# Performance work log

Hardware: AMD Instinct MI355X
Metric: run time of the kernel (lower is better)

Reference implementation:

```python
import jax, jax.numpy as jnp
import numpy as np

WBITS = 4   # weight bits (symmetric signed)
ABITS = 4   # activation bits (unsigned, [0,1])
CBITS = 4   # partial-sum quantization bits
ARRAY = 128 # crossbar array size (input-dim tile)
BN_EPS = 1e-5


def ste_round(x):
    # straight-through estimator round (identity gradient)
    return x + jax.lax.stop_gradient(jnp.round(x) - x)


def setup_inputs() -> dict:
    key = jax.random.key(0)
    k1, k2 = jax.random.split(key)
    B, FIN, FOUT = 65536, 256, 256
    x = jax.random.uniform(k1, (B, FIN), dtype=jnp.float32)        # quantized-act range [0,1]
    weight = jax.random.normal(k2, (FOUT, FIN), dtype=jnp.float32) * 0.05
    gamma = jnp.ones((FOUT,), jnp.float32)
    beta = jnp.zeros((FOUT,), jnp.float32)
    return {"x": x, "weight": weight, "gamma": gamma, "beta": beta}


def reference(x, weight, gamma, beta):
    qmax_w = 2 ** (WBITS - 1) - 1          # 7
    qmax_a = 2 ** ABITS - 1                # 15

    # --- symmetric weight quantization to WBITS (integer levels) ---
    scale_w = jnp.max(jnp.abs(weight)) / qmax_w
    w_int = ste_round(jnp.clip(weight / scale_w, -qmax_w, qmax_w))  # [Fout, Fin]

    # --- unsigned activation quantization to ABITS (integer levels) ---
    x_int = ste_round(jnp.clip(x, 0.0, 1.0) * qmax_a)               # [B, Fin]

    # --- crossbar-tiled integer matmul with partial-sum quantization ---
    B, Fin = x.shape
    Fout = weight.shape[0]
    T = Fin // ARRAY
    xt = x_int.reshape(B, T, ARRAY)          # [B, T, A]
    wt = w_int.reshape(Fout, T, ARRAY)       # [Fout, T, A]
    psum = jnp.einsum('bta,ota->bto', xt, wt)  # integer partial sums, [B, T, Fout]

    # quantize each partial sum to CBITS levels over the full tile dynamic range
    pmax = float(ARRAY * qmax_a * qmax_w)
    step = (2.0 * pmax) / (2 ** CBITS - 1)
    psum_q = ste_round(psum / step) * step

    acc = psum_q.sum(axis=1) * (scale_w / qmax_a)   # dequantized linear output [B, Fout]

    # --- BatchNorm1d (training mode: batch statistics) ---
    mu = acc.mean(axis=0)
    var = acc.var(axis=0)
    y = (acc - mu) * jax.lax.rsqrt(var + BN_EPS) * gamma + beta

    # --- quantized clipped-ReLU activation to ABITS ---
    out = ste_round(jnp.clip(y, 0.0, 1.0) * qmax_a) / qmax_a
    return out
```

## Files before the change

kernel.cpp:

```cpp
#include <hip/hip_runtime.h>
#include <cstdint>
#include <cstddef>

typedef int   v4i __attribute__((ext_vector_type(4)));
typedef float v4f __attribute__((ext_vector_type(4)));

static constexpr int NREP = 16;

static constexpr size_t WQ_OFF    = 0;
static constexpr size_t STATS_OFF = 65536;
static constexpr size_t PART_OFF  = STATS_OFF + NREP*512*4;
static constexpr size_t AB_OFF    = PART_OFF + 256;
static constexpr size_t SBUF_OFF  = 131072 + 2048;
static constexpr size_t WS_NEEDED = SBUF_OFF + (size_t)65536 * 256;

__device__ __forceinline__ int rhe1792(int p) {
    unsigned u = (unsigned)(p + 17024);
    unsigned v = u >> 8;
    unsigned d = (v * 147u) >> 10;
    int q = (int)d - 9;
    unsigned tie = (unsigned)(((u & 255u) | (v - 7u * d)) == 0u);
    q -= (int)(tie & ((unsigned)q & 1u));
    return q;
}

__global__ void k_maxabs(const float* __restrict__ w, float* __restrict__ partials,
                         int* __restrict__ stats) {
    __shared__ float wmax[4];
    int idx = blockIdx.x * 256 + threadIdx.x;
    float4 f = ((const float4*)w)[idx];
    float m = fmaxf(fmaxf(fabsf(f.x), fabsf(f.y)), fmaxf(fabsf(f.z), fabsf(f.w)));
    #pragma unroll
    for (int s = 32; s > 0; s >>= 1) m = fmaxf(m, __shfl_xor(m, s, 64));
    if ((threadIdx.x & 63) == 0) wmax[threadIdx.x >> 6] = m;
    if (idx < NREP * 512) stats[idx] = 0;
    __syncthreads();
    if (threadIdx.x == 0)
        partials[blockIdx.x] = fmaxf(fmaxf(wmax[0], wmax[1]), fmaxf(wmax[2], wmax[3]));
}

__device__ __forceinline__ float reduce_partials(const float* __restrict__ partials, int tid) {
    float p = partials[tid & 63];
    #pragma unroll
    for (int s = 32; s > 0; s >>= 1) p = fmaxf(p, __shfl_xor(p, s, 64));
    return p;
}

__global__ void k_wquant(const float* __restrict__ w, const float* __restrict__ partials,
                         signed char* __restrict__ wq) {
    int idx = blockIdx.x * 256 + threadIdx.x;
    float scale = reduce_partials(partials, threadIdx.x) / 7.0f;
    float4 f = ((const float4*)w)[idx];
    int q0 = (int)rintf(fminf(fmaxf(f.x / scale, -7.f), 7.f));
    int q1 = (int)rintf(fminf(fmaxf(f.y / scale, -7.f), 7.f));
    int q2 = (int)rintf(fminf(fmaxf(f.z / scale, -7.f), 7.f));
    int q3 = (int)rintf(fminf(fmaxf(f.w / scale, -7.f), 7.f));
    ((int*)wq)[idx] = (q0 & 255) | ((q1 & 255) << 8) | ((q2 & 255) << 16) | ((q3 & 255) << 24);
}

template <typename ST>
__global__ __launch_bounds__(256, 3) void k_gemm(
    const float* __restrict__ x, const signed char* __restrict__ wq,
    ST* __restrict__ sbuf, int* __restrict__ stats)
{
    __shared__ __align__(16) signed char ldsx[64 * 272];
    const int tid  = threadIdx.x;
    const int lane = tid & 63;
    const int wv   = tid >> 6;
    const int obase = wv * 64;
    const int lr = lane & 15, quad = lane >> 4;
    const size_t rb0 = (size_t)blockIdx.x * 64;

    v4f f[16];
    const v4f* xb = (const v4f*)(x + rb0 * 256);
    #pragma unroll
    for (int j = 0; j < 16; ++j)
        f[j] = __builtin_nontemporal_load(&xb[j * 256 + tid]);

    v4i wf[4][4];
    #pragma unroll
    for (int ot = 0; ot < 4; ++ot)
        #pragma unroll
        for (int kt = 0; kt < 4; ++kt)
            wf[ot][kt] = *(const v4i*)(wq + (size_t)(obase + ot * 16 + lr) * 256 + kt * 64 + quad * 16);

    #pragma unroll
    for (int j = 0; j < 16; ++j) {
        int idx = j * 256 + tid;
        int row = idx >> 6, c = idx & 63;
        int b0 = (int)rintf(fminf(fmaxf(f[j][0], 0.f), 1.f) * 15.f);
        int b1 = (int)rintf(fminf(fmaxf(f[j][1], 0.f), 1.f) * 15.f);
        int b2 = (int)rintf(fminf(fmaxf(f[j][2], 0.f), 1.f) * 15.f);
        int b3 = (int)rintf(fminf(fmaxf(f[j][3], 0.f), 1.f) * 15.f);
        *(int*)(ldsx + row * 272 + c * 4) = b0 | (b1 << 8) | (b2 << 16) | (b3 << 24);
    }
    __syncthreads();

    int ssum[4] = {0, 0, 0, 0};
    int ssq[4]  = {0, 0, 0, 0};

    #pragma unroll
    for (int t = 0; t < 4; ++t) {
        v4i a[4];
        #pragma unroll
        for (int kt = 0; kt < 4; ++kt)
            a[kt] = *(const v4i*)(ldsx + (t * 16 + lr) * 272 + kt * 64 + quad * 16);
        const size_t rowbase = rb0 + (size_t)t * 16;
        #pragma unroll
        for (int ot = 0; ot < 4; ++ot) {
            v4i acc0 = {0, 0, 0, 0}, acc1 = {0, 0, 0, 0};
            acc0 = __builtin_amdgcn_mfma_i32_16x16x64_i8(a[0], wf[ot][0], acc0, 0, 0, 0);
            acc0 = __builtin_amdgcn_mfma_i32_16x16x64_i8(a[1], wf[ot][1], acc0, 0, 0, 0);
            acc1 = __builtin_amdgcn_mfma_i32_16x16x64_i8(a[2], wf[ot][2], acc1, 0, 0, 0);
            acc1 = __builtin_amdgcn_mfma_i32_16x16x64_i8(a[3], wf[ot][3], acc1, 0, 0, 0);
            const int ocol = obase + ot * 16 + lr;
            ST* sp = sbuf + (rowbase + quad * 4) * 256 + ocol;
            #pragma unroll
            for (int e = 0; e < 4; ++e) {
                int s = rhe1792(acc0[e]) + rhe1792(acc1[e]);
                ssum[ot] += s;
                ssq[ot]  += s * s;
                sp[(size_t)e * 256] = (ST)s;
            }
        }
    }
    int* st = stats + (blockIdx.x & (NREP - 1)) * 512;
    #pragma unroll
    for (int ot = 0; ot < 4; ++ot) {
        int v = ssum[ot], u = ssq[ot];
        v += __shfl_xor(v, 16, 64); v += __shfl_xor(v, 32, 64);
        u += __shfl_xor(u, 16, 64); u += __shfl_xor(u, 32, 64);
        if (quad == 0) {
            atomicAdd(&st[obase + ot * 16 + lr], v);
            atomicAdd(&st[256 + obase + ot * 16 + lr], u);
        }
    }
}

__global__ void k_stats(const int* __restrict__ stats, const float* __restrict__ partials,
                        const float* __restrict__ gamma, const float* __restrict__ beta,
                        float2* __restrict__ AB)
{
    int o = threadIdx.x;
    int s = 0, q = 0;
    #pragma unroll
    for (int rr = 0; rr < NREP; ++rr) {
        s += stats[rr * 512 + o];
        q += stats[rr * 512 + 256 + o];
    }
    float scale_w = reduce_partials(partials, o) / 7.0f;
    float t = scale_w / 15.0f;
    double Cs = 1792.0 * (double)t;
    const double N = 65536.0;
    double mean_s = (double)s / N;
    double var_s  = (double)q / N - mean_s * mean_s;
    double var    = Cs * Cs * var_s;
    double inv    = 1.0 / sqrt(var + 1e-5);
    double A = Cs * inv * (double)gamma[o];
    double B = (double)beta[o] - Cs * mean_s * inv * (double)gamma[o];
    AB[o] = make_float2((float)A, (float)B);
}

template <typename LT>
__global__ __launch_bounds__(256) void k_out(const LT* sbuf, const float2* __restrict__ AB,
                                             float* out)
{
    const int tid = threadIdx.x;
    const int o0 = (tid * 4) & 255;
    const float4 ab01 = *(const float4*)((const float*)AB + 2 * o0);
    const float4 ab23 = *(const float4*)((const float*)AB + 2 * o0 + 4);
    const size_t base = (size_t)blockIdx.x * 1024 + tid;
    #pragma unroll
    for (int j = 0; j < 4; ++j) {
        const size_t F4 = base + (size_t)j * 256;
        float v0, v1, v2, v3;
        if constexpr (sizeof(LT) == 1) {
            int sv = ((const int*)sbuf)[F4];
            v0 = (float)((sv << 24) >> 24);
            v1 = (float)((sv << 16) >> 24);
            v2 = (float)((sv << 8) >> 24);
            v3 = (float)(sv >> 24);
        } else {
            v4f fl = ((const v4f*)sbuf)[F4];
            v0 = fl[0]; v1 = fl[1]; v2 = fl[2]; v3 = fl[3];
        }
        float y0 = rintf(fminf(fmaxf(v0 * ab01.x + ab01.y, 0.f), 1.f) * 15.f);
        float y1 = rintf(fminf(fmaxf(v1 * ab01.z + ab01.w, 0.f), 1.f) * 15.f);
        float y2 = rintf(fminf(fmaxf(v2 * ab23.x + ab23.y, 0.f), 1.f) * 15.f);
        float y3 = rintf(fminf(fmaxf(v3 * ab23.z + ab23.w, 0.f), 1.f) * 15.f);
        const float inv15 = 0.066666666666666666f;
        v4f o = { y0 * inv15, y1 * inv15, y2 * inv15, y3 * inv15 };
        __builtin_nontemporal_store(o, (v4f*)out + F4);
    }
}

extern "C" void kernel_launch(void* const* d_in, const int* in_sizes, int n_in,
                              void* d_out, int out_size, void* d_ws, size_t ws_size,
                              hipStream_t stream)
{
    const float* x     = (const float*)d_in[0];
    const float* w     = (const float*)d_in[1];
    const float* gamma = (const float*)d_in[2];
    const float* beta  = (const float*)d_in[3];
    float* out = (float*)d_out;
    char* ws = (char*)d_ws;

    signed char* wq       = (signed char*)(ws + WQ_OFF);
    int*         stats    = (int*)(ws + STATS_OFF);
    float*       partials = (float*)(ws + PART_OFF);
    float2*      AB       = (float2*)(ws + AB_OFF);

    k_maxabs<<<dim3(64), dim3(256), 0, stream>>>(w, partials, stats);
    k_wquant<<<dim3(64), dim3(256), 0, stream>>>(w, partials, wq);

    if (ws_size >= WS_NEEDED) {
        signed char* sbuf = (signed char*)(ws + SBUF_OFF);
        k_gemm<signed char><<<dim3(1024), dim3(256), 0, stream>>>(x, wq, sbuf, stats);
        k_stats<<<dim3(1), dim3(256), 0, stream>>>(stats, partials, gamma, beta, AB);
        k_out<signed char><<<dim3(4096), dim3(256), 0, stream>>>(sbuf, AB, out);
    } else {
        k_gemm<float><<<dim3(1024), dim3(256), 0, stream>>>(x, wq, out, stats);
        k_stats<<<dim3(1), dim3(256), 0, stream>>>(stats, partials, gamma, beta, AB);
        k_out<float><<<dim3(4096), dim3(256), 0, stream>>>(out, AB, out);
    }
}
```

Baseline: 142.1 us.

## Fuse BN stats finalize into GEMM via last-wave counter and halve row tile

Removes the separate single-block k_stats launch. Every wave of the GEMM now increments a global counter, and the last one computes the per-channel BN scale and shift from the accumulated stats. The GEMM row tile per block drops from 64 to 32, so the grid doubles to 2048 blocks, the LDS footprint halves and launch bounds rise to 4 blocks per CU. The MFMA accumulation now reuses one accumulator register set and interleaves rounding. This saves a kernel launch and dependency bubble, but adds an atomic per wave, a serialized tail reduction done by a single wave, and twice as many weight-fragment loads in total.

```diff
diff --git a/kernel.cpp b/kernel.cpp
--- a/kernel.cpp
+++ b/kernel.cpp
@@ -6,11 +6,13 @@
 typedef float v4f __attribute__((ext_vector_type(4)));
 
 static constexpr int NREP = 16;
+static constexpr unsigned WAVE_TOTAL = 2048u * 4u;
 
 static constexpr size_t WQ_OFF    = 0;
 static constexpr size_t STATS_OFF = 65536;
 static constexpr size_t PART_OFF  = STATS_OFF + NREP*512*4;
-static constexpr size_t AB_OFF    = PART_OFF + 256;
+static constexpr size_t CNT_OFF   = PART_OFF + 256;
+static constexpr size_t AB_OFF    = CNT_OFF + 64;
 static constexpr size_t SBUF_OFF  = 131072 + 2048;
 static constexpr size_t WS_NEEDED = SBUF_OFF + (size_t)65536 * 256;
 
@@ -25,7 +27,7 @@
 }
 
 __global__ void k_maxabs(const float* __restrict__ w, float* __restrict__ partials,
-                         int* __restrict__ stats) {
+                         int* __restrict__ stats, unsigned* __restrict__ counter) {
     __shared__ float wmax[4];
     int idx = blockIdx.x * 256 + threadIdx.x;
     float4 f = ((const float4*)w)[idx];
@@ -34,6 +36,7 @@
     for (int s = 32; s > 0; s >>= 1) m = fmaxf(m, __shfl_xor(m, s, 64));
     if ((threadIdx.x & 63) == 0) wmax[threadIdx.x >> 6] = m;
     if (idx < NREP * 512) stats[idx] = 0;
+    if (idx == 0) *counter = 0u;
     __syncthreads();
     if (threadIdx.x == 0)
         partials[blockIdx.x] = fmaxf(fmaxf(wmax[0], wmax[1]), fmaxf(wmax[2], wmax[3]));
@@ -59,22 +62,25 @@
 }
 
 template <typename ST>
-__global__ __launch_bounds__(256, 3) void k_gemm(
+__global__ __launch_bounds__(256, 4) void k_gemm(
     const float* __restrict__ x, const signed char* __restrict__ wq,
-    ST* __restrict__ sbuf, int* __restrict__ stats)
+    ST* __restrict__ sbuf, int* __restrict__ stats,
+    const float* __restrict__ partials, unsigned* __restrict__ counter,
+    const float* __restrict__ gamma, const float* __restrict__ beta,
+    float2* __restrict__ AB)
 {
-    __shared__ __align__(16) signed char ldsx[64 * 272];
+    __shared__ __align__(16) signed char ldsx[32 * 272];
     const int tid  = threadIdx.x;
     const int lane = tid & 63;
     const int wv   = tid >> 6;
     const int obase = wv * 64;
     const int lr = lane & 15, quad = lane >> 4;
-    const size_t rb0 = (size_t)blockIdx.x * 64;
-
-    v4f f[16];
+    const size_t rb0 = (size_t)blockIdx.x * 32;
+
+    v4f f[8];
     const v4f* xb = (const v4f*)(x + rb0 * 256);
     #pragma unroll
-    for (int j = 0; j < 16; ++j)
+    for (int j = 0; j < 8; ++j)
         f[j] = __builtin_nontemporal_load(&xb[j * 256 + tid]);
 
     v4i wf[4][4];
@@ -85,7 +91,7 @@
             wf[ot][kt] = *(const v4i*)(wq + (size_t)(obase + ot * 16 + lr) * 256 + kt * 64 + quad * 16);
 
     #pragma unroll
-    for (int j = 0; j < 16; ++j) {
+    for (int j = 0; j < 8; ++j) {
         int idx = j * 256 + tid;
         int row = idx >> 6, c = idx & 63;
         int b0 = (int)rintf(fminf(fmaxf(f[j][0], 0.f), 1.f) * 15.f);
@@ -100,7 +106,7 @@
     int ssq[4]  = {0, 0, 0, 0};
 
     #pragma unroll
-    for (int t = 0; t < 4; ++t) {
+    for (int t = 0; t < 2; ++t) {
         v4i a[4];
         #pragma unroll
         for (int kt = 0; kt < 4; ++kt)
@@ -108,16 +114,19 @@
         const size_t rowbase = rb0 + (size_t)t * 16;
         #pragma unroll
         for (int ot = 0; ot < 4; ++ot) {
-            v4i acc0 = {0, 0, 0, 0}, acc1 = {0, 0, 0, 0};
-            acc0 = __builtin_amdgcn_mfma_i32_16x16x64_i8(a[0], wf[ot][0], acc0, 0, 0, 0);
-            acc0 = __builtin_amdgcn_mfma_i32_16x16x64_i8(a[1], wf[ot][1], acc0, 0, 0, 0);
-            acc1 = __builtin_amdgcn_mfma_i32_16x16x64_i8(a[2], wf[ot][2], acc1, 0, 0, 0);
-            acc1 = __builtin_amdgcn_mfma_i32_16x16x64_i8(a[3], wf[ot][3], acc1, 0, 0, 0);
-            const int ocol = obase + ot * 16 + lr;
-            ST* sp = sbuf + (rowbase + quad * 4) * 256 + ocol;
+            v4i acc = {0, 0, 0, 0};
+            acc = __builtin_amdgcn_mfma_i32_16x16x64_i8(a[0], wf[ot][0], acc, 0, 0, 0);
+            acc = __builtin_amdgcn_mfma_i32_16x16x64_i8(a[1], wf[ot][1], acc, 0, 0, 0);
+            int q0[4];
+            #pragma unroll
+            for (int e = 0; e < 4; ++e) q0[e] = rhe1792(acc[e]);
+            acc = v4i{0, 0, 0, 0};
+            acc = __builtin_amdgcn_mfma_i32_16x16x64_i8(a[2], wf[ot][2], acc, 0, 0, 0);
+            acc = __builtin_amdgcn_mfma_i32_16x16x64_i8(a[3], wf[ot][3], acc, 0, 0, 0);
+            ST* sp = sbuf + (rowbase + quad * 4) * 256 + obase + ot * 16 + lr;
             #pragma unroll
             for (int e = 0; e < 4; ++e) {
-                int s = rhe1792(acc0[e]) + rhe1792(acc1[e]);
+                int s = q0[e] + rhe1792(acc[e]);
                 ssum[ot] += s;
                 ssq[ot]  += s * s;
                 sp[(size_t)e * 256] = (ST)s;
@@ -135,30 +144,38 @@
             atomicAdd(&st[256 + obase + ot * 16 + lr], u);
         }
     }
-}
-
-__global__ void k_stats(const int* __restrict__ stats, const float* __restrict__ partials,
-                        const float* __restrict__ gamma, const float* __restrict__ beta,
-                        float2* __restrict__ AB)
-{
-    int o = threadIdx.x;
-    int s = 0, q = 0;
-    #pragma unroll
-    for (int rr = 0; rr < NREP; ++rr) {
-        s += stats[rr * 512 + o];
-        q += stats[rr * 512 + 256 + o];
-    }
-    float scale_w = reduce_partials(partials, o) / 7.0f;
-    float t = scale_w / 15.0f;
-    double Cs = 1792.0 * (double)t;
-    const double N = 65536.0;
-    double mean_s = (double)s / N;
-    double var_s  = (double)q / N - mean_s * mean_s;
-    double var    = Cs * Cs * var_s;
-    double inv    = 1.0 / sqrt(var + 1e-5);
-    double A = Cs * inv * (double)gamma[o];
-    double B = (double)beta[o] - Cs * mean_s * inv * (double)gamma[o];
-    AB[o] = make_float2((float)A, (float)B);
+    unsigned r = 0;
+    if (lane == 0)
+        r = __hip_atomic_fetch_add(counter, 1u, __ATOMIC_ACQ_REL, __HIP_MEMORY_SCOPE_AGENT);
+    int isLast = __shfl((lane == 0 && r == WAVE_TOTAL - 1) ? 1 : 0, 0, 64);
+    if (isLast) {
+        float pm = __uint_as_float(__hip_atomic_load((const unsigned*)&partials[lane],
+                                   __ATOMIC_RELAXED, __HIP_MEMORY_SCOPE_AGENT));
+        #pragma unroll
+        for (int s = 32; s > 0; s >>= 1) pm = fmaxf(pm, __shfl_xor(pm, s, 64));
+        float scale_w = pm / 7.0f;
+        float tt = scale_w / 15.0f;
+        double Cs = 1792.0 * (double)tt;
+        const double N = 65536.0;
+        #pragma unroll
+        for (int c = 0; c < 4; ++c) {
+            int o = lane + 64 * c;
+            int s = 0, q = 0;
+            #pragma unroll
+            for (int rr = 0; rr < NREP; ++rr) {
+                s += __hip_atomic_load(&stats[rr * 512 + o],
+                                       __ATOMIC_RELAXED, __HIP_MEMORY_SCOPE_AGENT);
+                q += __hip_atomic_load(&stats[rr * 512 + 256 + o],
+                                       __ATOMIC_RELAXED, __HIP_MEMORY_SCOPE_AGENT);
+            }
+            double mean_s = (double)s / N;
+            double var_s  = (double)q / N - mean_s * mean_s;
+            double inv    = 1.0 / sqrt(Cs * Cs * var_s + 1e-5);
+            double A = Cs * inv * (double)gamma[o];
+            double B = (double)beta[o] - Cs * mean_s * inv * (double)gamma[o];
+            AB[o] = make_float2((float)A, (float)B);
+        }
+    }
 }
 
 template <typename LT>
@@ -208,19 +225,20 @@
     signed char* wq       = (signed char*)(ws + WQ_OFF);
     int*         stats    = (int*)(ws + STATS_OFF);
     float*       partials = (float*)(ws + PART_OFF);
+    unsigned*    counter  = (unsigned*)(ws + CNT_OFF);
     float2*      AB       = (float2*)(ws + AB_OFF);
 
-    k_maxabs<<<dim3(64), dim3(256), 0, stream>>>(w, partials, stats);
+    k_maxabs<<<dim3(64), dim3(256), 0, stream>>>(w, partials, stats, counter);
     k_wquant<<<dim3(64), dim3(256), 0, stream>>>(w, partials, wq);
 
     if (ws_size >= WS_NEEDED) {
         signed char* sbuf = (signed char*)(ws + SBUF_OFF);
-        k_gemm<signed char><<<dim3(1024), dim3(256), 0, stream>>>(x, wq, sbuf, stats);
-        k_stats<<<dim3(1), dim3(256), 0, stream>>>(stats, partials, gamma, beta, AB);
+        k_gemm<signed char><<<dim3(2048), dim3(256), 0, stream>>>(
+            x, wq, sbuf, stats, partials, counter, gamma, beta, AB);
         k_out<signed char><<<dim3(4096), dim3(256), 0, stream>>>(sbuf, AB, out);
     } else {
-        k_gemm<float><<<dim3(1024), dim3(256), 0, stream>>>(x, wq, out, stats);
-        k_stats<<<dim3(1), dim3(256), 0, stream>>>(stats, partials, gamma, beta, AB);
+        k_gemm<float><<<dim3(2048), dim3(256), 0, stream>>>(
+            x, wq, out, stats, partials, counter, gamma, beta, AB);
         k_out<float><<<dim3(4096), dim3(256), 0, stream>>>(out, AB, out);
     }
 }
```

Result: slower. 449.8 us (+216.6%).
